# Performance work log

Measured on AMD Instinct MI355X. Metric: run time of the kernel, lower is better.

Reference implementation:

```python
import jax, jax.numpy as jnp
import numpy as np

B, C, H, W = 8, 8, 512, 512

# one-pixel shifts with zero padding (equivalent to the bmm with shift matrices)
def shift_right(x):  # out[..., c] = x[..., c-1]
    return jnp.pad(x, ((0, 0), (0, 0), (1, 0)))[:, :, :-1]
def shift_left(x):   # out[..., c] = x[..., c+1]
    return jnp.pad(x, ((0, 0), (0, 0), (0, 1)))[:, :, 1:]
def shift_up(x):     # out[r] = x[r+1]
    return jnp.pad(x, ((0, 0), (0, 1), (0, 0)))[:, 1:, :]
def shift_down(x):   # out[r] = x[r-1]
    return jnp.pad(x, ((0, 0), (1, 0), (0, 0)))[:, :-1, :]

def bilater_voting(c):
    # c: [B, 8, H, W] probabilities
    right        = shift_right(c[:, 4])
    left         = shift_left(c[:, 3])
    left_bottom  = shift_left(shift_down(c[:, 5]))
    right_above  = shift_right(shift_up(c[:, 2]))
    left_above   = shift_left(shift_up(c[:, 0]))
    bottom       = shift_down(c[:, 6])
    up           = shift_up(c[:, 1])
    right_bottom = shift_right(shift_down(c[:, 7]))
    a1 = c[:, 3] * right
    a2 = c[:, 4] * left
    a3 = c[:, 1] * bottom
    a4 = c[:, 6] * up
    a5 = c[:, 2] * left_bottom
    a6 = c[:, 5] * right_above
    a7 = c[:, 0] * right_bottom
    a8 = c[:, 7] * left_above
    vote_out = jnp.stack([a7, a3, a5, a1, a2, a6, a4, a8], axis=1)
    glo_map = jnp.mean(vote_out, axis=1)
    return glo_map, vote_out

def bce(p, t):
    # matches torch F.binary_cross_entropy (mean reduction, log clamped at -100)
    logp = jnp.clip(jnp.log(p), -100.0, None)
    log1mp = jnp.clip(jnp.log(1.0 - p), -100.0, None)
    return -jnp.mean(t * logp + (1.0 - t) * log1mp)

def setup_inputs() -> dict:
    key = jax.random.key(0)
    k1, k2, k3, k4 = jax.random.split(key, 4)
    atts = jax.random.normal(k1, (B, C, H, W), dtype=jnp.float32)
    dets = jax.random.normal(k2, (B, C, H, W), dtype=jnp.float32)
    target = jax.random.randint(k3, (B, 1, H, W), 0, 2).astype(jnp.float32)
    con_target = jax.random.randint(k4, (B, C, H, W), 0, 2).astype(jnp.float32)
    return {"atts": atts, "dets": dets, "target": target, "con_target": con_target}

def reference(atts, dets, target, con_target):
    # edge mask from connectivity GT: pixels with 0 < sum < 8
    sum_conn = jnp.sum(con_target, axis=1)  # [B, H, W]
    edge_conn = jnp.where((sum_conn < 8.0) & (sum_conn > 0.0), 1.0, 0.0)

    atts_p = jax.nn.sigmoid(atts)
    dets_p = jax.nn.sigmoid(dets)

    glo_map1, vote_out1 = bilater_voting(atts_p)
    glo_map2, vote_out2 = bilater_voting(dets_p)

    # edge/decouple loss on dets branch
    pred_mask_min = 1.0 - jnp.min(vote_out2, axis=1)
    pred_mask_min = pred_mask_min * edge_conn
    decouple_map = glo_map2 * (1.0 - edge_conn) + pred_mask_min
    de_loss2 = bce(decouple_map[:, None], target)

    bce_loss1 = bce(glo_map1[:, None], target)
    bicon_loss1 = bce(vote_out1, con_target)
    conn_loss1 = bce(atts_p, con_target)
    bicon_loss2 = bce(vote_out2, con_target)
    conn_loss2 = bce(dets_p, con_target)

    loss = (0.2 * bicon_loss1 + 0.8 * conn_loss1 + bce_loss1
            + 0.2 * bicon_loss2 + 0.8 * conn_loss2 + de_loss2)
    return loss
```

## Files before the change

### kernel.cpp

```cpp
#include <hip/hip_runtime.h>

#define BB 8
#define CC 8
#define HH 512
#define WW 512
#define HWSZ (HH * WW)
#define CHW (CC * HWSZ)

typedef float v4 __attribute__((ext_vector_type(4)));

#define LOG2_CLAMP -144.26950409f

__device__ __forceinline__ float sigf(float x) {
    return __builtin_amdgcn_rcpf(1.0f + __expf(-x));
}

template <bool NEED_MIN>
__device__ __forceinline__ void eval_branch(
    const float* __restrict__ Lb, const float* __restrict__ craw,
    int w, int wl, int wr, float mh0, float mh1, float mw0, float mw1,
    const float* __restrict__ cv,
    float& glo, float& vmin, float& Lbic, float& Lcon)
{
    float s[8];
#pragma unroll
    for (int c = 0; c < 8; ++c) s[c] = sigf(craw[c]);

    float n[8];
    n[0] = sigf(Lb[4 * WW + wl]) * (mh0 * mw0);
    n[1] = sigf(Lb[3 * WW + w ]) *  mh0;
    n[2] = sigf(Lb[2 * WW + wr]) * (mh0 * mw1);
    n[3] = sigf(Lb[1 * WW + wl]) *  mw0;
    n[4] = sigf(Lb[0 * WW + wr]) *  mw1;
    n[5] = sigf(Lb[7 * WW + wl]) * (mh1 * mw0);
    n[6] = sigf(Lb[6 * WW + w ]) *  mh1;
    n[7] = sigf(Lb[5 * WW + wr]) * (mh1 * mw1);

    float pb0 = 1.f, pb1 = 1.f, pc = 1.f, vsum = 0.f;
    if (NEED_MIN) vmin = 1e30f;
#pragma unroll
    for (int k = 0; k < 8; ++k) {
        float v = s[k] * n[k];
        vsum += v;
        if (NEED_MIN) vmin = fminf(vmin, v);
        float t  = cv[k];
        float av = (t > 0.5f) ? v    : 1.0f - v;
        float as = (t > 0.5f) ? s[k] : 1.0f - s[k];
        if (k < 4) pb0 *= av; else pb1 *= av;
        pc *= as;
    }
    glo  = vsum * 0.125f;
    Lbic = fmaxf(__log2f(pb0), LOG2_CLAMP) + fmaxf(__log2f(pb1), LOG2_CLAMP);
    Lcon = fmaxf(__log2f(pc), LOG2_CLAMP);
}

__global__ __launch_bounds__(512, 8) void bicon_loss_kernel(
    const float* __restrict__ atts, const float* __restrict__ dets,
    const float* __restrict__ target, const float* __restrict__ con,
    float* __restrict__ out)
{
    __shared__ float L[16 * WW];
    __shared__ float wsum[8];

    const int t   = threadIdx.x;
    const int row = blockIdx.x;
    const int h   = row & (HH - 1);
    const int b   = row >> 9;
    const int w   = t;

    const int   hm  = (h > 0)      ? h - 1 : 0;
    const int   hp  = (h < HH - 1) ? h + 1 : HH - 1;
    const float mh0 = (h > 0)      ? 1.0f : 0.0f;
    const float mh1 = (h < HH - 1) ? 1.0f : 0.0f;
    const int   wl  = (w > 0)      ? w - 1 : 0;
    const int   wr  = (w < WW - 1) ? w + 1 : WW - 1;
    const float mw0 = (w > 0)      ? 1.0f : 0.0f;
    const float mw1 = (w < WW - 1) ? 1.0f : 0.0f;

    const float* __restrict__ ab = atts + b * CHW;
    const float* __restrict__ db = dets + b * CHW;
    const int offC = h * WW + w;

    const int rgrp = t >> 7;
    const int col4 = (t & 127) << 2;

    v4 stg[4];
#pragma unroll
    for (int j = 0; j < 4; ++j) {
        const int rr = rgrp + 4 * (j & 1);
        const int ch   = (rr < 5) ? rr + 3 : rr - 5;
        const int grow = (rr < 2) ? h : ((rr < 5) ? hm : hp);
        const float* base = (j < 2) ? ab : db;
        stg[j] = *(const v4* __restrict__)(base + ch * HWSZ + grow * WW + col4);
    }

    float cv[8];
#pragma unroll
    for (int c = 0; c < 8; ++c) cv[c] = con[b * CHW + c * HWSZ + offC];
    const float tt = target[b * HWSZ + offC];
    float ar[8], dr[8];
#pragma unroll
    for (int c = 0; c < 8; ++c) ar[c] = ab[c * HWSZ + offC];
#pragma unroll
    for (int c = 0; c < 8; ++c) dr[c] = db[c * HWSZ + offC];

#pragma unroll
    for (int j = 0; j < 4; ++j) {
        const int r = rgrp + 4 * (j & 1) + ((j < 2) ? 0 : 8);
        *(v4*)(L + r * WW + col4) = stg[j];
    }
    __syncthreads();

    float glo1, glo2, vmin2, dum, Lb1, Lc1, Lb2, Lc2;
    eval_branch<false>(L,           ar, w, wl, wr, mh0, mh1, mw0, mw1, cv,
                       glo1, dum, Lb1, Lc1);
    eval_branch<true >(L + 8 * WW,  dr, w, wl, wr, mh0, mh1, mw0, mw1, cv,
                       glo2, vmin2, Lb2, Lc2);

    float csum = 0.f;
#pragma unroll
    for (int c = 0; c < 8; ++c) csum += cv[c];
    const float edge = (csum < 8.0f && csum > 0.0f) ? 1.0f : 0.0f;

    const float dec = (edge > 0.5f) ? (1.0f - vmin2) : glo2;
    const float a   = (tt > 0.5f) ? glo1 : 1.0f - glo1;
    const float bs  = (tt > 0.5f) ? dec  : 1.0f - dec;
    const float Lp  = fmaxf(__log2f(a * bs), LOG2_CLAMP);

    const float wbic = 0.2f / (float)(BB * CC * HWSZ);
    const float wcon = 0.8f / (float)(BB * CC * HWSZ);
    const float wpix = 1.0f / (float)(BB * HWSZ);
    const float ln2  = 0.69314718056f;

    float local = -(wbic * (Lb1 + Lb2) + wcon * (Lc1 + Lc2) + wpix * Lp) * ln2;

#pragma unroll
    for (int off = 32; off > 0; off >>= 1)
        local += __shfl_down(local, off, 64);

    const int lane = t & 63;
    const int wid  = t >> 6;
    if (lane == 0) wsum[wid] = local;
    __syncthreads();
    if (t == 0) {
        float s = 0.f;
#pragma unroll
        for (int i = 0; i < 8; ++i) s += wsum[i];
        atomicAdd(out, s);
    }
}

extern "C" void kernel_launch(void* const* d_in, const int* in_sizes, int n_in,
                              void* d_out, int out_size, void* d_ws, size_t ws_size,
                              hipStream_t stream) {
    const float* atts   = (const float*)d_in[0];
    const float* dets   = (const float*)d_in[1];
    const float* target = (const float*)d_in[2];
    const float* con    = (const float*)d_in[3];
    float* out = (float*)d_out;

    hipMemsetAsync(out, 0, sizeof(float), stream);

    bicon_loss_kernel<<<BB * HH, 512, 0, stream>>>(atts, dets, target, con, out);
}
```

Measured before the change: 206.0 us.

## Process eight rows per block with double-buffered async LDS staging and prefetch

Each block now handles eight consecutive rows instead of one. The neighbour rows are staged into a double-buffered LDS array with global_load_lds direct-to-LDS loads, and the centre-pixel values for the next row are prefetched into registers while the current row is computed. The centre channels 3 and 4 are read from the staged LDS rows rather than loaded again from global memory. The aim is to hide memory latency and cut redundant loads, at the cost of double the LDS per block, a smaller grid and a lower launch-bounds occupancy target.

```diff
diff --git a/kernel.cpp b/kernel.cpp
--- a/kernel.cpp
+++ b/kernel.cpp
@@ -6,6 +6,7 @@
 #define WW 512
 #define HWSZ (HH * WW)
 #define CHW (CC * HWSZ)
+#define RPB 8
 
 typedef float v4 __attribute__((ext_vector_type(4)));
 
@@ -15,16 +16,41 @@
     return __builtin_amdgcn_rcpf(1.0f + __expf(-x));
 }
 
+__device__ __forceinline__ void stage_glds(
+    const float* __restrict__ ab, const float* __restrict__ db,
+    float* __restrict__ Lbuf, int h, int hm, int hp, int wave, int lane)
+{
+#pragma unroll
+    for (int j = 0; j < 2; ++j) {
+        const int row = 2 * wave + j;
+        const int rr  = row & 7;
+        const int ch  = (rr < 5) ? rr + 3 : rr - 5;
+        const int gr  = (rr < 2) ? h : ((rr < 5) ? hm : hp);
+        const float* gbase = ((row < 8) ? ab : db) + ch * HWSZ + gr * WW;
+#pragma unroll
+        for (int k = 0; k < 2; ++k) {
+            const float* g = gbase + k * 256 + lane * 4;
+            float* l = Lbuf + row * WW + k * 256;
+            __builtin_amdgcn_global_load_lds(
+                (const __attribute__((address_space(1))) unsigned int*)g,
+                (__attribute__((address_space(3))) unsigned int*)l,
+                16, 0, 0);
+        }
+    }
+}
+
 template <bool NEED_MIN>
 __device__ __forceinline__ void eval_branch(
-    const float* __restrict__ Lb, const float* __restrict__ craw,
+    const float* __restrict__ Lb, const float* __restrict__ cr6,
     int w, int wl, int wr, float mh0, float mh1, float mw0, float mw1,
     const float* __restrict__ cv,
     float& glo, float& vmin, float& Lbic, float& Lcon)
 {
     float s[8];
-#pragma unroll
-    for (int c = 0; c < 8; ++c) s[c] = sigf(craw[c]);
+    s[0] = sigf(cr6[0]); s[1] = sigf(cr6[1]); s[2] = sigf(cr6[2]);
+    s[3] = sigf(Lb[0 * WW + w]);
+    s[4] = sigf(Lb[1 * WW + w]);
+    s[5] = sigf(cr6[3]); s[6] = sigf(cr6[4]); s[7] = sigf(cr6[5]);
 
     float n[8];
     n[0] = sigf(Lb[4 * WW + wl]) * (mh0 * mw0);
@@ -54,93 +80,119 @@
     Lcon = fmaxf(__log2f(pc), LOG2_CLAMP);
 }
 
-__global__ __launch_bounds__(512, 8) void bicon_loss_kernel(
+__global__ __launch_bounds__(512, 4) void bicon_loss_kernel(
     const float* __restrict__ atts, const float* __restrict__ dets,
     const float* __restrict__ target, const float* __restrict__ con,
     float* __restrict__ out)
 {
-    __shared__ float L[16 * WW];
+    __shared__ float L[2][16 * WW];
     __shared__ float wsum[8];
 
-    const int t   = threadIdx.x;
-    const int row = blockIdx.x;
-    const int h   = row & (HH - 1);
-    const int b   = row >> 9;
-    const int w   = t;
-
-    const int   hm  = (h > 0)      ? h - 1 : 0;
-    const int   hp  = (h < HH - 1) ? h + 1 : HH - 1;
-    const float mh0 = (h > 0)      ? 1.0f : 0.0f;
-    const float mh1 = (h < HH - 1) ? 1.0f : 0.0f;
+    const int t    = threadIdx.x;
+    const int lane = t & 63;
+    const int wave = t >> 6;
+    const int w    = t;
+
     const int   wl  = (w > 0)      ? w - 1 : 0;
     const int   wr  = (w < WW - 1) ? w + 1 : WW - 1;
     const float mw0 = (w > 0)      ? 1.0f : 0.0f;
     const float mw1 = (w < WW - 1) ? 1.0f : 0.0f;
 
-    const float* __restrict__ ab = atts + b * CHW;
-    const float* __restrict__ db = dets + b * CHW;
-    const int offC = h * WW + w;
-
-    const int rgrp = t >> 7;
-    const int col4 = (t & 127) << 2;
-
-    v4 stg[4];
-#pragma unroll
-    for (int j = 0; j < 4; ++j) {
-        const int rr = rgrp + 4 * (j & 1);
-        const int ch   = (rr < 5) ? rr + 3 : rr - 5;
-        const int grow = (rr < 2) ? h : ((rr < 5) ? hm : hp);
-        const float* base = (j < 2) ? ab : db;
-        stg[j] = *(const v4* __restrict__)(base + ch * HWSZ + grow * WW + col4);
-    }
-
-    float cv[8];
-#pragma unroll
-    for (int c = 0; c < 8; ++c) cv[c] = con[b * CHW + c * HWSZ + offC];
-    const float tt = target[b * HWSZ + offC];
-    float ar[8], dr[8];
-#pragma unroll
-    for (int c = 0; c < 8; ++c) ar[c] = ab[c * HWSZ + offC];
-#pragma unroll
-    for (int c = 0; c < 8; ++c) dr[c] = db[c * HWSZ + offC];
-
-#pragma unroll
-    for (int j = 0; j < 4; ++j) {
-        const int r = rgrp + 4 * (j & 1) + ((j < 2) ? 0 : 8);
-        *(v4*)(L + r * WW + col4) = stg[j];
-    }
-    __syncthreads();
-
-    float glo1, glo2, vmin2, dum, Lb1, Lc1, Lb2, Lc2;
-    eval_branch<false>(L,           ar, w, wl, wr, mh0, mh1, mw0, mw1, cv,
-                       glo1, dum, Lb1, Lc1);
-    eval_branch<true >(L + 8 * WW,  dr, w, wl, wr, mh0, mh1, mw0, mw1, cv,
-                       glo2, vmin2, Lb2, Lc2);
-
-    float csum = 0.f;
-#pragma unroll
-    for (int c = 0; c < 8; ++c) csum += cv[c];
-    const float edge = (csum < 8.0f && csum > 0.0f) ? 1.0f : 0.0f;
-
-    const float dec = (edge > 0.5f) ? (1.0f - vmin2) : glo2;
-    const float a   = (tt > 0.5f) ? glo1 : 1.0f - glo1;
-    const float bs  = (tt > 0.5f) ? dec  : 1.0f - dec;
-    const float Lp  = fmaxf(__log2f(a * bs), LOG2_CLAMP);
+    const int row0 = blockIdx.x * RPB;
+
+    {
+        const int h  = row0 & (HH - 1);
+        const int b  = row0 >> 9;
+        const int hm = (h > 0) ? h - 1 : 0;
+        const int hp = (h < HH - 1) ? h + 1 : HH - 1;
+        stage_glds(atts + b * CHW, dets + b * CHW, L[0], h, hm, hp, wave, lane);
+    }
+    float pfA[6], pfD[6], pfC[8], pfT;
+    {
+        const int h = row0 & (HH - 1);
+        const int b = row0 >> 9;
+        const int off = h * WW + w;
+        const float* __restrict__ ab = atts + b * CHW + off;
+        const float* __restrict__ db = dets + b * CHW + off;
+        const float* __restrict__ cb = con  + b * CHW + off;
+        const int chn[6] = {0, 1, 2, 5, 6, 7};
+#pragma unroll
+        for (int i = 0; i < 6; ++i) pfA[i] = ab[chn[i] * HWSZ];
+#pragma unroll
+        for (int i = 0; i < 6; ++i) pfD[i] = db[chn[i] * HWSZ];
+#pragma unroll
+        for (int c = 0; c < 8; ++c) pfC[c] = cb[c * HWSZ];
+        pfT = target[b * HWSZ + off];
+    }
 
     const float wbic = 0.2f / (float)(BB * CC * HWSZ);
     const float wcon = 0.8f / (float)(BB * CC * HWSZ);
     const float wpix = 1.0f / (float)(BB * HWSZ);
     const float ln2  = 0.69314718056f;
 
-    float local = -(wbic * (Lb1 + Lb2) + wcon * (Lc1 + Lc2) + wpix * Lp) * ln2;
+    float acc = 0.0f;
+
+    for (int r = 0; r < RPB; ++r) {
+        __syncthreads();
+
+        float cA[6], cD[6], cC[8];
+#pragma unroll
+        for (int i = 0; i < 6; ++i) { cA[i] = pfA[i]; cD[i] = pfD[i]; }
+#pragma unroll
+        for (int c = 0; c < 8; ++c) cC[c] = pfC[c];
+        const float cT = pfT;
+
+        const int grow = row0 + r;
+        const int h    = grow & (HH - 1);
+        const float mh0 = (h > 0) ? 1.0f : 0.0f;
+        const float mh1 = (h < HH - 1) ? 1.0f : 0.0f;
+
+        if (r + 1 < RPB) {
+            const int g2 = grow + 1;
+            const int h2 = g2 & (HH - 1);
+            const int b2 = g2 >> 9;
+            const int hm2 = (h2 > 0) ? h2 - 1 : 0;
+            const int hp2 = (h2 < HH - 1) ? h2 + 1 : HH - 1;
+            stage_glds(atts + b2 * CHW, dets + b2 * CHW, L[(r + 1) & 1],
+                       h2, hm2, hp2, wave, lane);
+            const int off2 = h2 * WW + w;
+            const float* __restrict__ ab = atts + b2 * CHW + off2;
+            const float* __restrict__ db = dets + b2 * CHW + off2;
+            const float* __restrict__ cb = con  + b2 * CHW + off2;
+            const int chn[6] = {0, 1, 2, 5, 6, 7};
+#pragma unroll
+            for (int i = 0; i < 6; ++i) pfA[i] = ab[chn[i] * HWSZ];
+#pragma unroll
+            for (int i = 0; i < 6; ++i) pfD[i] = db[chn[i] * HWSZ];
+#pragma unroll
+            for (int c = 0; c < 8; ++c) pfC[c] = cb[c * HWSZ];
+            pfT = target[b2 * HWSZ + off2];
+        }
+
+        const float* __restrict__ Lc = L[r & 1];
+        float glo1, glo2, vmin2, dum, Lb1, Lc1, Lb2, Lc2;
+        eval_branch<false>(Lc,          cA, w, wl, wr, mh0, mh1, mw0, mw1, cC,
+                           glo1, dum, Lb1, Lc1);
+        eval_branch<true >(Lc + 8 * WW, cD, w, wl, wr, mh0, mh1, mw0, mw1, cC,
+                           glo2, vmin2, Lb2, Lc2);
+
+        float csum = 0.f;
+#pragma unroll
+        for (int c = 0; c < 8; ++c) csum += cC[c];
+        const float edge = (csum < 8.0f && csum > 0.0f) ? 1.0f : 0.0f;
+
+        const float dec = (edge > 0.5f) ? (1.0f - vmin2) : glo2;
+        const float a   = (cT > 0.5f) ? glo1 : 1.0f - glo1;
+        const float bs  = (cT > 0.5f) ? dec  : 1.0f - dec;
+        const float Lp  = fmaxf(__log2f(a * bs), LOG2_CLAMP);
+
+        acc += -(wbic * (Lb1 + Lb2) + wcon * (Lc1 + Lc2) + wpix * Lp) * ln2;
+    }
 
 #pragma unroll
     for (int off = 32; off > 0; off >>= 1)
-        local += __shfl_down(local, off, 64);
-
-    const int lane = t & 63;
-    const int wid  = t >> 6;
-    if (lane == 0) wsum[wid] = local;
+        acc += __shfl_down(acc, off, 64);
+    if (lane == 0) wsum[wave] = acc;
     __syncthreads();
     if (t == 0) {
         float s = 0.f;
@@ -161,5 +213,5 @@
 
     hipMemsetAsync(out, 0, sizeof(float), stream);
 
-    bicon_loss_kernel<<<BB * HH, 512, 0, stream>>>(atts, dets, target, con, out);
-}
+    bicon_loss_kernel<<<(BB * HH) / RPB, 512, 0, stream>>>(atts, dets, target, con, out);
+}
```

Measured after the change: 215.2 us. 1.04x slower.

## Sweep multiple rows per block with rolling register window and prefetch

Applied to the files above, without the earlier changes.

Each block now processes 16 consecutive rows, keeping the previous, current and next rows' sigmoids in registers and prefetching the row after next while computing. Neighbour values are exchanged via double-buffered LDS with a single barrier per row. This removes the redundant halo reloads and repeated sigmoid evaluation across per-row blocks. The cost is far fewer blocks (one per CU), which may limit occupancy and memory parallelism, plus heavier register use.

```diff
diff --git a/kernel.cpp b/kernel.cpp
--- a/kernel.cpp
+++ b/kernel.cpp
@@ -6,8 +6,7 @@
 #define WW 512
 #define HWSZ (HH * WW)
 #define CHW (CC * HWSZ)
-
-typedef float v4 __attribute__((ext_vector_type(4)));
+#define RR 16
 
 #define LOG2_CLAMP -144.26950409f
 
@@ -15,37 +14,56 @@
     return __builtin_amdgcn_rcpf(1.0f + __expf(-x));
 }
 
+__device__ __forceinline__ void lds_barrier() {
+    __builtin_amdgcn_s_waitcnt(0xC07F);
+    __builtin_amdgcn_s_barrier();
+}
+
+struct Raw { float a[8]; float d[8]; float c[8]; float t; };
+
+__device__ __forceinline__ void issue_bundle(
+    Raw& r,
+    const float* const* __restrict__ Ap, const float* const* __restrict__ Dp,
+    const float* const* __restrict__ Cp, const float* __restrict__ Tp,
+    int grow, int w)
+{
+    const int off = grow * WW + w;
+#pragma unroll
+    for (int ch = 0; ch < 8; ++ch) r.a[ch] = Ap[ch][off];
+#pragma unroll
+    for (int ch = 0; ch < 8; ++ch) r.d[ch] = Dp[ch][off];
+#pragma unroll
+    for (int ch = 0; ch < 8; ++ch) r.c[ch] = Cp[ch][off];
+    r.t = Tp[off];
+}
+
 template <bool NEED_MIN>
-__device__ __forceinline__ void eval_branch(
-    const float* __restrict__ Lb, const float* __restrict__ craw,
-    int w, int wl, int wr, float mh0, float mh1, float mw0, float mw1,
-    const float* __restrict__ cv,
+__device__ __forceinline__ void votes_branch(
+    const float* __restrict__ Lb,
+    const float* sp, const float* sC, const float* sN, const float* cv,
+    int wl, int wr, float mh0, float mh1, float mw0, float mw1,
     float& glo, float& vmin, float& Lbic, float& Lcon)
 {
-    float s[8];
-#pragma unroll
-    for (int c = 0; c < 8; ++c) s[c] = sigf(craw[c]);
-
     float n[8];
-    n[0] = sigf(Lb[4 * WW + wl]) * (mh0 * mw0);
-    n[1] = sigf(Lb[3 * WW + w ]) *  mh0;
-    n[2] = sigf(Lb[2 * WW + wr]) * (mh0 * mw1);
-    n[3] = sigf(Lb[1 * WW + wl]) *  mw0;
-    n[4] = sigf(Lb[0 * WW + wr]) *  mw1;
-    n[5] = sigf(Lb[7 * WW + wl]) * (mh1 * mw0);
-    n[6] = sigf(Lb[6 * WW + w ]) *  mh1;
-    n[7] = sigf(Lb[5 * WW + wr]) * (mh1 * mw1);
+    n[0] = Lb[1 * WW + wl] * (mh0 * mw0);
+    n[1] = sp[6]           *  mh0;
+    n[2] = Lb[0 * WW + wr] * (mh0 * mw1);
+    n[3] = Lb[3 * WW + wl] *  mw0;
+    n[4] = Lb[2 * WW + wr] *  mw1;
+    n[5] = Lb[5 * WW + wl] * (mh1 * mw0);
+    n[6] = sN[1]           *  mh1;
+    n[7] = Lb[4 * WW + wr] * (mh1 * mw1);
 
     float pb0 = 1.f, pb1 = 1.f, pc = 1.f, vsum = 0.f;
     if (NEED_MIN) vmin = 1e30f;
 #pragma unroll
     for (int k = 0; k < 8; ++k) {
-        float v = s[k] * n[k];
+        float v = sC[k] * n[k];
         vsum += v;
         if (NEED_MIN) vmin = fminf(vmin, v);
         float t  = cv[k];
-        float av = (t > 0.5f) ? v    : 1.0f - v;
-        float as = (t > 0.5f) ? s[k] : 1.0f - s[k];
+        float av = (t > 0.5f) ? v     : 1.0f - v;
+        float as = (t > 0.5f) ? sC[k] : 1.0f - sC[k];
         if (k < 4) pb0 *= av; else pb1 *= av;
         pc *= as;
     }
@@ -54,93 +72,120 @@
     Lcon = fmaxf(__log2f(pc), LOG2_CLAMP);
 }
 
-__global__ __launch_bounds__(512, 8) void bicon_loss_kernel(
+__global__ __launch_bounds__(512, 2) void bicon_loss_kernel(
     const float* __restrict__ atts, const float* __restrict__ dets,
     const float* __restrict__ target, const float* __restrict__ con,
     float* __restrict__ out)
 {
-    __shared__ float L[16 * WW];
+    __shared__ float Lds[2][12 * WW];
     __shared__ float wsum[8];
 
-    const int t   = threadIdx.x;
-    const int row = blockIdx.x;
-    const int h   = row & (HH - 1);
-    const int b   = row >> 9;
-    const int w   = t;
-
-    const int   hm  = (h > 0)      ? h - 1 : 0;
-    const int   hp  = (h < HH - 1) ? h + 1 : HH - 1;
-    const float mh0 = (h > 0)      ? 1.0f : 0.0f;
-    const float mh1 = (h < HH - 1) ? 1.0f : 0.0f;
+    const int t  = threadIdx.x;
+    const int w  = t;
+    const int b  = blockIdx.x >> 5;
+    const int h0 = (blockIdx.x & 31) * RR;
+
     const int   wl  = (w > 0)      ? w - 1 : 0;
     const int   wr  = (w < WW - 1) ? w + 1 : WW - 1;
     const float mw0 = (w > 0)      ? 1.0f : 0.0f;
     const float mw1 = (w < WW - 1) ? 1.0f : 0.0f;
 
-    const float* __restrict__ ab = atts + b * CHW;
-    const float* __restrict__ db = dets + b * CHW;
-    const int offC = h * WW + w;
-
-    const int rgrp = t >> 7;
-    const int col4 = (t & 127) << 2;
-
-    v4 stg[4];
-#pragma unroll
-    for (int j = 0; j < 4; ++j) {
-        const int rr = rgrp + 4 * (j & 1);
-        const int ch   = (rr < 5) ? rr + 3 : rr - 5;
-        const int grow = (rr < 2) ? h : ((rr < 5) ? hm : hp);
-        const float* base = (j < 2) ? ab : db;
-        stg[j] = *(const v4* __restrict__)(base + ch * HWSZ + grow * WW + col4);
-    }
-
-    float cv[8];
-#pragma unroll
-    for (int c = 0; c < 8; ++c) cv[c] = con[b * CHW + c * HWSZ + offC];
-    const float tt = target[b * HWSZ + offC];
-    float ar[8], dr[8];
-#pragma unroll
-    for (int c = 0; c < 8; ++c) ar[c] = ab[c * HWSZ + offC];
-#pragma unroll
-    for (int c = 0; c < 8; ++c) dr[c] = db[c * HWSZ + offC];
-
-#pragma unroll
-    for (int j = 0; j < 4; ++j) {
-        const int r = rgrp + 4 * (j & 1) + ((j < 2) ? 0 : 8);
-        *(v4*)(L + r * WW + col4) = stg[j];
-    }
-    __syncthreads();
-
-    float glo1, glo2, vmin2, dum, Lb1, Lc1, Lb2, Lc2;
-    eval_branch<false>(L,           ar, w, wl, wr, mh0, mh1, mw0, mw1, cv,
-                       glo1, dum, Lb1, Lc1);
-    eval_branch<true >(L + 8 * WW,  dr, w, wl, wr, mh0, mh1, mw0, mw1, cv,
-                       glo2, vmin2, Lb2, Lc2);
-
-    float csum = 0.f;
-#pragma unroll
-    for (int c = 0; c < 8; ++c) csum += cv[c];
-    const float edge = (csum < 8.0f && csum > 0.0f) ? 1.0f : 0.0f;
-
-    const float dec = (edge > 0.5f) ? (1.0f - vmin2) : glo2;
-    const float a   = (tt > 0.5f) ? glo1 : 1.0f - glo1;
-    const float bs  = (tt > 0.5f) ? dec  : 1.0f - dec;
-    const float Lp  = fmaxf(__log2f(a * bs), LOG2_CLAMP);
+    const float* Ap[8]; const float* Dp[8]; const float* Cp[8];
+#pragma unroll
+    for (int ch = 0; ch < 8; ++ch) {
+        Ap[ch] = atts + (long)b * CHW + (long)ch * HWSZ;
+        Dp[ch] = dets + (long)b * CHW + (long)ch * HWSZ;
+        Cp[ch] = con  + (long)b * CHW + (long)ch * HWSZ;
+    }
+    const float* Tp = target + (long)b * HWSZ;
+
+    Raw r0, r1, r2;
+    issue_bundle(r0, Ap, Dp, Cp, Tp, (h0 > 0) ? h0 - 1 : 0, w);
+    issue_bundle(r1, Ap, Dp, Cp, Tp, h0, w);
+    issue_bundle(r2, Ap, Dp, Cp, Tp, h0 + 1, w);
+
+    float spA[8], spD[8], sCA[8], sCD[8], cvC[8], tgtC;
+#pragma unroll
+    for (int ch = 0; ch < 8; ++ch) { spA[ch] = sigf(r0.a[ch]); spD[ch] = sigf(r0.d[ch]); }
+#pragma unroll
+    for (int ch = 0; ch < 8; ++ch) { sCA[ch] = sigf(r1.a[ch]); sCD[ch] = sigf(r1.d[ch]); cvC[ch] = r1.c[ch]; }
+    tgtC = r1.t;
 
     const float wbic = 0.2f / (float)(BB * CC * HWSZ);
     const float wcon = 0.8f / (float)(BB * CC * HWSZ);
     const float wpix = 1.0f / (float)(BB * HWSZ);
-    const float ln2  = 0.69314718056f;
-
-    float local = -(wbic * (Lb1 + Lb2) + wcon * (Lc1 + Lc2) + wpix * Lp) * ln2;
+
+    float acc = 0.0f;
+    Raw rp = r2;
+
+#pragma unroll 4
+    for (int r = 0; r < RR; ++r) {
+        const int h = h0 + r;
+
+        Raw rnew = rp;
+        if (r < RR - 1) {
+            const int h2 = (h + 2 < HH) ? h + 2 : HH - 1;
+            issue_bundle(rnew, Ap, Dp, Cp, Tp, h2, w);
+        }
+
+        float sNA[8], sND[8], cvN[8];
+#pragma unroll
+        for (int ch = 0; ch < 8; ++ch) {
+            sNA[ch] = sigf(rp.a[ch]);
+            sND[ch] = sigf(rp.d[ch]);
+            cvN[ch] = rp.c[ch];
+        }
+        const float tgtN = rp.t;
+
+        float* __restrict__ Lb = Lds[r & 1];
+        Lb[ 0 * WW + w] = spA[5];  Lb[ 1 * WW + w] = spA[7];
+        Lb[ 2 * WW + w] = sCA[3];  Lb[ 3 * WW + w] = sCA[4];
+        Lb[ 4 * WW + w] = sNA[0];  Lb[ 5 * WW + w] = sNA[2];
+        Lb[ 6 * WW + w] = spD[5];  Lb[ 7 * WW + w] = spD[7];
+        Lb[ 8 * WW + w] = sCD[3];  Lb[ 9 * WW + w] = sCD[4];
+        Lb[10 * WW + w] = sND[0];  Lb[11 * WW + w] = sND[2];
+
+        lds_barrier();
+
+        const float mh0 = (h > 0)      ? 1.0f : 0.0f;
+        const float mh1 = (h < HH - 1) ? 1.0f : 0.0f;
+
+        float glo1, glo2, vmin2, dum, Lb1, Lc1, Lb2, Lc2;
+        votes_branch<false>(Lb,          spA, sCA, sNA, cvC, wl, wr,
+                            mh0, mh1, mw0, mw1, glo1, dum, Lb1, Lc1);
+        votes_branch<true >(Lb + 6 * WW, spD, sCD, sND, cvC, wl, wr,
+                            mh0, mh1, mw0, mw1, glo2, vmin2, Lb2, Lc2);
+
+        float csum = 0.f;
+#pragma unroll
+        for (int ch = 0; ch < 8; ++ch) csum += cvC[ch];
+        const float edge = (csum < 8.0f && csum > 0.0f) ? 1.0f : 0.0f;
+
+        const float dec = (edge > 0.5f) ? (1.0f - vmin2) : glo2;
+        const float pa  = (tgtC > 0.5f) ? glo1 : 1.0f - glo1;
+        const float pb  = (tgtC > 0.5f) ? dec  : 1.0f - dec;
+        const float Lp  = fmaxf(__log2f(pa * pb), LOG2_CLAMP);
+
+        acc += wbic * (Lb1 + Lb2) + wcon * (Lc1 + Lc2) + wpix * Lp;
+
+#pragma unroll
+        for (int ch = 0; ch < 8; ++ch) {
+            spA[ch] = sCA[ch];  spD[ch] = sCD[ch];
+            sCA[ch] = sNA[ch];  sCD[ch] = sND[ch];
+            cvC[ch] = cvN[ch];
+        }
+        tgtC = tgtN;
+        rp = rnew;
+    }
+
+    acc *= -0.69314718056f;
 
 #pragma unroll
     for (int off = 32; off > 0; off >>= 1)
-        local += __shfl_down(local, off, 64);
-
+        acc += __shfl_down(acc, off, 64);
     const int lane = t & 63;
     const int wid  = t >> 6;
-    if (lane == 0) wsum[wid] = local;
+    if (lane == 0) wsum[wid] = acc;
     __syncthreads();
     if (t == 0) {
         float s = 0.f;
@@ -161,5 +206,5 @@
 
     hipMemsetAsync(out, 0, sizeof(float), stream);
 
-    bicon_loss_kernel<<<BB * HH, 512, 0, stream>>>(atts, dets, target, con, out);
-}
+    bicon_loss_kernel<<<BB * (HH / RR), 512, 0, stream>>>(atts, dets, target, con, out);
+}
```

Result: no change. 209.7 us (+1.8%).
